# Performance work log

Measured on AMD Instinct MI355X. Metric: run time of the kernel, lower is better.

Reference implementation:

```python
import jax, jax.numpy as jnp
import numpy as np

P, B, FEAT, HID, ATTN, NHEAD = 4096, 32, 512, 512, 512, 8
HD = ATTN // NHEAD  # 64


def setup_inputs() -> dict:
    key = jax.random.key(0)
    ks = jax.random.split(key, 12)
    s = lambda n: 1.0 / np.sqrt(n)
    return {
        "last_hidden": jax.random.normal(ks[0], (1, B, HID), jnp.float32),
        "encoder_outputs": jax.random.normal(ks[1], (P, B, FEAT), jnp.float32),
        # outer projections (stored [in, out]; torch Linear is x @ W.T + b)
        "Wa_w": jax.random.uniform(ks[2], (FEAT, ATTN), jnp.float32, -s(FEAT), s(FEAT)),
        "Wa_b": jax.random.uniform(ks[3], (ATTN,), jnp.float32, -s(FEAT), s(FEAT)),
        "Ua_w": jax.random.uniform(ks[4], (HID, ATTN), jnp.float32, -s(HID), s(HID)),
        "Ua_b": jax.random.uniform(ks[5], (ATTN,), jnp.float32, -s(HID), s(HID)),
        # inner Attention(head_attn_size, head_attn_size, head_attn_size)
        "Wa2_w": jax.random.uniform(ks[6], (HD, HD), jnp.float32, -s(HD), s(HD)),
        "Wa2_b": jax.random.uniform(ks[7], (HD,), jnp.float32, -s(HD), s(HD)),
        "Ua2_w": jax.random.uniform(ks[8], (HD, HD), jnp.float32, -s(HD), s(HD)),
        "Ua2_b": jax.random.uniform(ks[9], (HD,), jnp.float32, -s(HD), s(HD)),
        "va_w": jax.random.uniform(ks[10], (HD, 1), jnp.float32, -s(HD), s(HD)),
        "va_b": jax.random.uniform(ks[11], (1,), jnp.float32, -s(HD), s(HD)),
        "nhead": NHEAD,
    }


def reference(last_hidden, encoder_outputs, Wa_w, Wa_b, Ua_w, Ua_b,
              Wa2_w, Wa2_b, Ua2_w, Ua2_b, va_w, va_b, nhead):
    p, b = encoder_outputs.shape[:2]
    enc = encoder_outputs @ Wa_w + Wa_b            # [P,B,A]
    hid = last_hidden @ Ua_w + Ua_b                # [1,B,A]
    hd = enc.shape[-1] // nhead
    enc = enc.reshape(p, b, nhead, hd)             # [P,B,nh,hd]
    hid = hid.reshape(1, b, nhead, hd)             # [1,B,nh,hd]
    # inner Bahdanau attention
    a = jnp.tanh((enc @ Wa2_w + Wa2_b) + (hid @ Ua2_w + Ua2_b))
    scores = a @ va_w + va_b                       # [P,B,nh,1]
    weights = jax.nn.softmax(scores, axis=0)       # softmax over pixels
    context = jnp.sum(weights * enc, axis=0, keepdims=True)  # [1,B,nh,hd]
    weight = jnp.mean(weights, axis=-2)            # mean over heads -> [P,B,1]
    context = context.reshape(1, b, nhead * hd)    # [1,B,A]
    return context, weight
```

## Files before the change

### kernel.cpp

```cpp
#include <hip/hip_runtime.h>
#include <hip/hip_bf16.h>

#define PDIM 4096
#define BDIM 32
#define MDIM (PDIM*BDIM)
#define KDIM 512
#define NDIM 512
#define NH   8
#define HD   64

typedef __attribute__((ext_vector_type(4))) float f32x4;
typedef __attribute__((ext_vector_type(8))) short bf16x8;

__device__ __forceinline__ unsigned short f2bf(float f) {
  unsigned u = __float_as_uint(f);
  u += 0x7fffu + ((u >> 16) & 1u);
  return (unsigned short)(u >> 16);
}
__device__ __forceinline__ float bf2f(unsigned short u) {
  return __uint_as_float(((unsigned)u) << 16);
}

__device__ __forceinline__ float fast_tanh(float x) {
  x = fminf(fmaxf(x, -15.f), 15.f);
  float e = __expf(2.f * x);
  return __fdividef(e - 1.f, e + 1.f);
}

#define GLOAD_LDS16(g, l) __builtin_amdgcn_global_load_lds( \
    (const __attribute__((address_space(1))) void*)(g),     \
    (__attribute__((address_space(3))) void*)(l), 16, 0, 0)

__global__ __launch_bounds__(256) void cvt_k(
    const float* __restrict__ x, unsigned short* __restrict__ xbf) {
  size_t i = ((size_t)blockIdx.x * 256 + threadIdx.x) * 8;
  float4 a = *(const float4*)(x + i);
  float4 b = *(const float4*)(x + i + 4);
  ushort4 o0; o0.x = f2bf(a.x); o0.y = f2bf(a.y); o0.z = f2bf(a.z); o0.w = f2bf(a.w);
  ushort4 o1; o1.x = f2bf(b.x); o1.y = f2bf(b.y); o1.z = f2bf(b.z); o1.w = f2bf(b.w);
  *(ushort4*)(xbf + i) = o0;
  *(ushort4*)(xbf + i + 4) = o1;
}

__global__ __launch_bounds__(512) void hub_k(
    const float* __restrict__ lh, const float* __restrict__ Ua,
    const float* __restrict__ Ua_b, const float* __restrict__ Ua2,
    const float* __restrict__ Ua2_b, const float* __restrict__ Wa_b,
    const float* __restrict__ Wa2, const float* __restrict__ Wa2_b,
    float* __restrict__ ubf) {
  int b = blockIdx.x, tid = threadIdx.x;
  __shared__ float ls[512];
  __shared__ float hs[512];
  ls[tid] = lh[b*512 + tid];
  __syncthreads();
  float s = Ua_b[tid];
  #pragma unroll 8
  for (int k = 0; k < 512; ++k)
    s += ls[k] * Ua[(size_t)k*512 + tid];
  hs[tid] = s;
  __syncthreads();
  int h = tid >> 6, j = tid & 63;
  float u = Ua2_b[j] + Wa2_b[j];
  #pragma unroll 4
  for (int k = 0; k < 64; ++k) {
    u += hs[h*64 + k] * Ua2[k*64 + j];
    u += Wa_b[h*64 + k] * Wa2[k*64 + j];
  }
  ubf[b*512 + tid] = u;
}

__global__ __launch_bounds__(256) void wft_k(
    const float* __restrict__ Wa, const float* __restrict__ Wa2,
    unsigned short* __restrict__ WfT) {
  int n = blockIdx.x, tid = threadIdx.x;
  int h = n >> 6, j = n & 63;
  __shared__ float w2[64];
  if (tid < 64) w2[tid] = Wa2[tid*64 + j];
  __syncthreads();
  for (int k = tid; k < 512; k += 256) {
    float s = 0.f;
    #pragma unroll 8
    for (int kk = 0; kk < 64; ++kk)
      s += Wa[(size_t)k*512 + h*64 + kk] * w2[kk];
    WfT[(size_t)n*512 + k] = f2bf(s);
  }
}

__global__ __launch_bounds__(256, 4) void gemm_score_k(
    const unsigned short* __restrict__ xbf, const unsigned short* __restrict__ WfT,
    const float* __restrict__ ubf, const float* __restrict__ va_w,
    const float* __restrict__ va_b, float* __restrict__ scores) {
  __shared__ __align__(16) unsigned short As[8192];
  __shared__ __align__(16) unsigned short Bs[8192];
  int tid = threadIdx.x;
  int bn = blockIdx.x, bm = blockIdx.y;
  int m0 = bm*128, n0 = bn*128;
  int lane = tid & 63, w = tid >> 6;
  int quad = lane >> 4, l16 = lane & 15;
  int wr = w >> 1, wc = w & 1;
  f32x4 acc[4][4] = {};

  for (int k0 = 0; k0 < KDIM; k0 += 64) {
    __syncthreads();
    #pragma unroll
    for (int i = 0; i < 4; ++i) {
      int c = i*256 + tid;
      int r = c & 127, kc = c >> 7;
      GLOAD_LDS16(xbf + (size_t)(m0 + r)*512 + k0 + kc*8, As + (size_t)c*8);
    }
    #pragma unroll
    for (int i = 0; i < 4; ++i) {
      int c = i*256 + tid;
      int r = c & 127, kc = c >> 7;
      GLOAD_LDS16(WfT + (size_t)(n0 + r)*512 + k0 + kc*8, Bs + (size_t)c*8);
    }
    __syncthreads();
    #pragma unroll
    for (int kk = 0; kk < 64; kk += 32) {
      int kc = (kk >> 3) + quad;
      bf16x8 af[4], bfr[4];
      #pragma unroll
      for (int ti = 0; ti < 4; ++ti)
        af[ti] = *(const bf16x8*)(As + ((size_t)kc*128 + 64*wr + 16*ti + l16)*8);
      #pragma unroll
      for (int tj = 0; tj < 4; ++tj)
        bfr[tj] = *(const bf16x8*)(Bs + ((size_t)kc*128 + 64*wc + 16*tj + l16)*8);
      #pragma unroll
      for (int ti = 0; ti < 4; ++ti)
        #pragma unroll
        for (int tj = 0; tj < 4; ++tj)
          acc[ti][tj] = __builtin_amdgcn_mfma_f32_16x16x32_bf16(
              af[ti], bfr[tj], acc[ti][tj], 0, 0, 0);
    }
  }

  int head = bn*2 + wc;
  float va_r[4];
  #pragma unroll
  for (int tj = 0; tj < 4; ++tj) va_r[tj] = va_w[16*tj + l16];
  float vb = va_b[0];
  const float* ubf_col = ubf + n0 + 64*wc + l16;
  #pragma unroll
  for (int ti = 0; ti < 4; ++ti) {
    #pragma unroll
    for (int r = 0; r < 4; ++r) {
      int row_loc = 64*wr + 16*ti + 4*quad + r;
      int b31 = row_loc & 31;
      float s = 0.f;
      #pragma unroll
      for (int tj = 0; tj < 4; ++tj) {
        float xa = acc[ti][tj][r] + ubf_col[b31*512 + 16*tj];
        s += fast_tanh(xa) * va_r[tj];
      }
      s += __shfl_xor(s, 1); s += __shfl_xor(s, 2);
      s += __shfl_xor(s, 4); s += __shfl_xor(s, 8);
      if (l16 == 0)
        scores[(size_t)(head*32 + b31)*PDIM + bm*4 + (row_loc >> 5)] = s + vb;
    }
  }
}

__global__ __launch_bounds__(256) void softmax_k(
    const float* __restrict__ sc, float* __restrict__ w) {
  int row = blockIdx.x;
  int tid = threadIdx.x;
  const float* s = sc + (size_t)row*PDIM;
  float v[16];
  float mx = -1e30f;
  #pragma unroll
  for (int i = 0; i < 16; ++i) {
    v[i] = s[tid + i*256];
    mx = fmaxf(mx, v[i]);
  }
  for (int m = 1; m < 64; m <<= 1) mx = fmaxf(mx, __shfl_xor(mx, m));
  __shared__ float redm[4], reds[4];
  int wid = tid >> 6, lane = tid & 63;
  if (lane == 0) redm[wid] = mx;
  __syncthreads();
  mx = fmaxf(fmaxf(redm[0], redm[1]), fmaxf(redm[2], redm[3]));
  float sum = 0.f;
  #pragma unroll
  for (int i = 0; i < 16; ++i) { v[i] = __expf(v[i] - mx); sum += v[i]; }
  for (int m = 1; m < 64; m <<= 1) sum += __shfl_xor(sum, m);
  if (lane == 0) reds[wid] = sum;
  __syncthreads();
  sum = reds[0] + reds[1] + reds[2] + reds[3];
  float inv = 1.f / sum;
  #pragma unroll
  for (int i = 0; i < 16; ++i)
    w[(size_t)row*PDIM + tid + i*256] = v[i] * inv;
}

__global__ __launch_bounds__(256) void mean_k(
    const float* __restrict__ w, float* __restrict__ out) {
  int tid = threadIdx.x;
  int p0 = blockIdx.x * 32;
  int b = tid >> 3, j = tid & 7;
  float4 s = {0.f, 0.f, 0.f, 0.f};
  #pragma unroll
  for (int h = 0; h < NH; ++h) {
    float4 v = *(const float4*)(w + (size_t)(h*32 + b)*PDIM + p0 + j*4);
    s.x += v.x; s.y += v.y; s.z += v.z; s.w += v.w;
  }
  __shared__ float l[32][33];
  l[j*4+0][b] = s.x * 0.125f;
  l[j*4+1][b] = s.y * 0.125f;
  l[j*4+2][b] = s.z * 0.125f;
  l[j*4+3][b] = s.w * 0.125f;
  __syncthreads();
  float4 o;
  int mm = tid*4;
  o.x = l[(mm+0) >> 5][(mm+0) & 31];
  o.y = l[(mm+1) >> 5][(mm+1) & 31];
  o.z = l[(mm+2) >> 5][(mm+2) & 31];
  o.w = l[(mm+3) >> 5][(mm+3) & 31];
  *(float4*)(out + BDIM*NDIM + (size_t)p0*32 + mm) = o;
}

__global__ __launch_bounds__(256) void ctx_partial_k(
    const unsigned short* __restrict__ xbf, const float* __restrict__ w,
    float* __restrict__ part) {
  int pc = blockIdx.x;
  int b  = blockIdx.y;
  int tid = threadIdx.x;
  __shared__ float wl[8*256];
  __shared__ float red[4][512];
  {
    int hq = tid >> 5, l = tid & 31;
    const float* wrow = w + (size_t)(hq*32 + b)*PDIM + pc*256 + l*8;
    float4 a = ((const float4*)wrow)[0], c = ((const float4*)wrow)[1];
    float* dst = wl + hq*256 + l*8;
    ((float4*)dst)[0] = a; ((float4*)dst)[1] = c;
  }
  __syncthreads();
  int lane = tid & 63, wv = tid >> 6;
  float acc[8][8];
  #pragma unroll
  for (int h = 0; h < 8; ++h)
    #pragma unroll
    for (int j = 0; j < 8; ++j) acc[h][j] = 0.f;
  for (int i = 0; i < 64; ++i) {
    int pl = wv*64 + i;
    bf16x8 xv = *(const bf16x8*)(xbf + ((size_t)((pc*256 + pl)*32 + b))*512 + lane*8);
    float xf[8];
    #pragma unroll
    for (int j = 0; j < 8; ++j) xf[j] = bf2f((unsigned short)xv[j]);
    #pragma unroll
    for (int h = 0; h < 8; ++h) {
      float ww = wl[h*256 + pl];
      #pragma unroll
      for (int j = 0; j < 8; ++j) acc[h][j] += ww * xf[j];
    }
  }
  for (int h = 0; h < 8; ++h) {
    #pragma unroll
    for (int j = 0; j < 8; j += 4)
      *(float4*)(&red[wv][lane*8 + j]) = *(float4*)(&acc[h][j]);
    __syncthreads();
    if (tid < 64) {
      #pragma unroll
      for (int j = 0; j < 8; ++j) {
        int f = tid*8 + j;
        part[((size_t)(b*16 + pc)*NH + h)*512 + f] =
            red[0][f] + red[1][f] + red[2][f] + red[3][f];
      }
    }
    __syncthreads();
  }
}

__global__ __launch_bounds__(256) void ctx_reduce_k(
    const float* __restrict__ part, float* __restrict__ cx) {
  int gid = blockIdx.x*256 + threadIdx.x;
  int f = gid & 511;
  int bh = gid >> 9;
  int h = bh & 7, b = bh >> 3;
  float s = 0.f;
  #pragma unroll
  for (int pc = 0; pc < 16; ++pc)
    s += part[((size_t)(b*16 + pc)*NH + h)*512 + f];
  cx[gid] = s;
}

__global__ __launch_bounds__(256) void ctx_proj_k(
    const float* __restrict__ cx, const float* __restrict__ Wa,
    const float* __restrict__ Wa_b, float* __restrict__ out) {
  int b = blockIdx.x >> 3, h = blockIdx.x & 7;
  int tid = threadIdx.x;
  __shared__ float cs[512];
  cs[tid]       = cx[(size_t)blockIdx.x*512 + tid];
  cs[tid + 256] = cx[(size_t)blockIdx.x*512 + tid + 256];
  __syncthreads();
  int d = tid & 63, g = tid >> 6;
  float s = 0.f;
  #pragma unroll 8
  for (int f = g*128; f < g*128 + 128; ++f)
    s += cs[f] * Wa[(size_t)f*512 + h*64 + d];
  __shared__ float red[256];
  red[tid] = s;
  __syncthreads();
  if (tid < 64) {
    float tot = red[tid] + red[64+tid] + red[128+tid] + red[192+tid] + Wa_b[h*64 + tid];
    out[b*512 + h*64 + tid] = tot;
  }
}

extern "C" void kernel_launch(void* const* d_in, const int* in_sizes, int n_in,
                              void* d_out, int out_size, void* d_ws, size_t ws_size,
                              hipStream_t stream) {
  (void)in_sizes; (void)n_in; (void)out_size; (void)ws_size;
  const float* lh    = (const float*)d_in[0];
  const float* x     = (const float*)d_in[1];
  const float* Wa_w  = (const float*)d_in[2];
  const float* Wa_b  = (const float*)d_in[3];
  const float* Ua_w  = (const float*)d_in[4];
  const float* Ua_b  = (const float*)d_in[5];
  const float* Wa2_w = (const float*)d_in[6];
  const float* Wa2_b = (const float*)d_in[7];
  const float* Ua2_w = (const float*)d_in[8];
  const float* Ua2_b = (const float*)d_in[9];
  const float* va_w  = (const float*)d_in[10];
  const float* va_b  = (const float*)d_in[11];
  float* out = (float*)d_out;
  char* ws = (char*)d_ws;

  unsigned short* xbf = (unsigned short*)(ws);
  unsigned short* WfT = (unsigned short*)(ws + 134217728);
  float* ubf    = (float*)(ws + 134742016);
  float* scores = (float*)(ws + 134807552);
  float* w      = (float*)(ws + 139001856);
  float* part   = (float*)(ws + 143196160);
  float* cx     = (float*)(ws + 151584768);

  hipLaunchKernelGGL(cvt_k, dim3(32768), dim3(256), 0, stream, x, xbf);
  hipLaunchKernelGGL(hub_k, dim3(32), dim3(512), 0, stream,
                     lh, Ua_w, Ua_b, Ua2_w, Ua2_b, Wa_b, Wa2_w, Wa2_b, ubf);
  hipLaunchKernelGGL(wft_k, dim3(512), dim3(256), 0, stream, Wa_w, Wa2_w, WfT);
  hipLaunchKernelGGL(gemm_score_k, dim3(4, 1024), dim3(256), 0, stream,
                     xbf, WfT, ubf, va_w, va_b, scores);
  hipLaunchKernelGGL(softmax_k, dim3(256), dim3(256), 0, stream, scores, w);
  hipLaunchKernelGGL(mean_k, dim3(128), dim3(256), 0, stream, w, out);
  hipLaunchKernelGGL(ctx_partial_k, dim3(16, 32), dim3(256), 0, stream, xbf, w, part);
  hipLaunchKernelGGL(ctx_reduce_k, dim3(512), dim3(256), 0, stream, part, cx);
  hipLaunchKernelGGL(ctx_proj_k, dim3(256), dim3(256), 0, stream, cx, Wa_w, Wa_b, out);
}
```

Measured before the change: 674.2 us.

## Remap GEMM tiles to one batch per block, vectorize score stores, fuse ctx reduce

```diff
diff --git a/kernel.cpp b/kernel.cpp
--- a/kernel.cpp
+++ b/kernel.cpp
@@ -86,7 +86,7 @@
   }
 }
 
-__global__ __launch_bounds__(256, 4) void gemm_score_k(
+__global__ __launch_bounds__(256, 5) void gemm_score_k(
     const unsigned short* __restrict__ xbf, const unsigned short* __restrict__ WfT,
     const float* __restrict__ ubf, const float* __restrict__ va_w,
     const float* __restrict__ va_b, float* __restrict__ scores) {
@@ -94,11 +94,20 @@
   __shared__ __align__(16) unsigned short Bs[8192];
   int tid = threadIdx.x;
   int bn = blockIdx.x, bm = blockIdx.y;
-  int m0 = bm*128, n0 = bn*128;
+  int b = bm & 31, p0 = (bm >> 5) << 7;
+  int n0 = bn*128;
   int lane = tid & 63, w = tid >> 6;
   int quad = lane >> 4, l16 = lane & 15;
   int wr = w >> 1, wc = w & 1;
+  float va_r[4], ub_r[4];
+  #pragma unroll
+  for (int tj = 0; tj < 4; ++tj) {
+    va_r[tj] = va_w[16*tj + l16];
+    ub_r[tj] = ubf[b*512 + n0 + 64*wc + 16*tj + l16];
+  }
+  float vb = va_b[0];
   f32x4 acc[4][4] = {};
+  const unsigned short* abase = xbf + (size_t)p0*16384 + (size_t)b*512;
 
   for (int k0 = 0; k0 < KDIM; k0 += 64) {
     __syncthreads();
@@ -106,7 +115,7 @@
     for (int i = 0; i < 4; ++i) {
       int c = i*256 + tid;
       int r = c & 127, kc = c >> 7;
-      GLOAD_LDS16(xbf + (size_t)(m0 + r)*512 + k0 + kc*8, As + (size_t)c*8);
+      GLOAD_LDS16(abase + (size_t)r*16384 + k0 + kc*8, As + (size_t)c*8);
     }
     #pragma unroll
     for (int i = 0; i < 4; ++i) {
@@ -135,28 +144,23 @@
   }
 
   int head = bn*2 + wc;
-  float va_r[4];
-  #pragma unroll
-  for (int tj = 0; tj < 4; ++tj) va_r[tj] = va_w[16*tj + l16];
-  float vb = va_b[0];
-  const float* ubf_col = ubf + n0 + 64*wc + l16;
+  float* srow = scores + (size_t)(head*32 + b)*PDIM + p0;
   #pragma unroll
   for (int ti = 0; ti < 4; ++ti) {
+    float4 sv;
+    float* svp = &sv.x;
     #pragma unroll
     for (int r = 0; r < 4; ++r) {
-      int row_loc = 64*wr + 16*ti + 4*quad + r;
-      int b31 = row_loc & 31;
       float s = 0.f;
       #pragma unroll
-      for (int tj = 0; tj < 4; ++tj) {
-        float xa = acc[ti][tj][r] + ubf_col[b31*512 + 16*tj];
-        s += fast_tanh(xa) * va_r[tj];
-      }
+      for (int tj = 0; tj < 4; ++tj)
+        s += fast_tanh(acc[ti][tj][r] + ub_r[tj]) * va_r[tj];
       s += __shfl_xor(s, 1); s += __shfl_xor(s, 2);
       s += __shfl_xor(s, 4); s += __shfl_xor(s, 8);
-      if (l16 == 0)
-        scores[(size_t)(head*32 + b31)*PDIM + bm*4 + (row_loc >> 5)] = s + vb;
-    }
+      svp[r] = s + vb;
+    }
+    if (l16 == 0)
+      *(float4*)(srow + 64*wr + 16*ti + 4*quad) = sv;
   }
 }
 
@@ -269,27 +273,21 @@
   }
 }
 
-__global__ __launch_bounds__(256) void ctx_reduce_k(
-    const float* __restrict__ part, float* __restrict__ cx) {
-  int gid = blockIdx.x*256 + threadIdx.x;
-  int f = gid & 511;
-  int bh = gid >> 9;
-  int h = bh & 7, b = bh >> 3;
-  float s = 0.f;
-  #pragma unroll
-  for (int pc = 0; pc < 16; ++pc)
-    s += part[((size_t)(b*16 + pc)*NH + h)*512 + f];
-  cx[gid] = s;
-}
-
-__global__ __launch_bounds__(256) void ctx_proj_k(
-    const float* __restrict__ cx, const float* __restrict__ Wa,
+__global__ __launch_bounds__(256) void ctx_projred_k(
+    const float* __restrict__ part, const float* __restrict__ Wa,
     const float* __restrict__ Wa_b, float* __restrict__ out) {
-  int b = blockIdx.x >> 3, h = blockIdx.x & 7;
+  int bh = blockIdx.x;
+  int b = bh >> 3, h = bh & 7;
   int tid = threadIdx.x;
   __shared__ float cs[512];
-  cs[tid]       = cx[(size_t)blockIdx.x*512 + tid];
-  cs[tid + 256] = cx[(size_t)blockIdx.x*512 + tid + 256];
+  float s0 = 0.f, s1 = 0.f;
+  #pragma unroll
+  for (int pc = 0; pc < 16; ++pc) {
+    const float* pp = part + ((size_t)(b*16 + pc)*NH + h)*512;
+    s0 += pp[tid];
+    s1 += pp[tid + 256];
+  }
+  cs[tid] = s0; cs[tid + 256] = s1;
   __syncthreads();
   int d = tid & 63, g = tid >> 6;
   float s = 0.f;
@@ -330,7 +328,6 @@
   float* scores = (float*)(ws + 134807552);
   float* w      = (float*)(ws + 139001856);
   float* part   = (float*)(ws + 143196160);
-  float* cx     = (float*)(ws + 151584768);
 
   hipLaunchKernelGGL(cvt_k, dim3(32768), dim3(256), 0, stream, x, xbf);
   hipLaunchKernelGGL(hub_k, dim3(32), dim3(512), 0, stream,
@@ -341,6 +338,5 @@
   hipLaunchKernelGGL(softmax_k, dim3(256), dim3(256), 0, stream, scores, w);
   hipLaunchKernelGGL(mean_k, dim3(128), dim3(256), 0, stream, w, out);
   hipLaunchKernelGGL(ctx_partial_k, dim3(16, 32), dim3(256), 0, stream, xbf, w, part);
-  hipLaunchKernelGGL(ctx_reduce_k, dim3(512), dim3(256), 0, stream, part, cx);
-  hipLaunchKernelGGL(ctx_proj_k, dim3(256), dim3(256), 0, stream, cx, Wa_w, Wa_b, out);
-}
+  hipLaunchKernelGGL(ctx_projred_k, dim3(256), dim3(256), 0, stream, part, Wa_w, Wa_b, out);
+}
```

Measured after the change: 757.3 us. 1.12x slower.
